# Kernel optimization log

Hardware: AMD Instinct MI355X
Metric: run time of the kernel (lower is better)

Reference implementation:

```python
import jax, jax.numpy as jnp
import numpy as np

N = 50000        # number of nodes
K = 32           # sampled neighbors per node (fixed degree)
D = 128          # input_dim
DOUT = 128       # output_dim


def setup_inputs() -> dict:
    key = jax.random.key(0)
    k1, k2, k3, k4, k5 = jax.random.split(key, 5)
    node_fea1 = jax.random.normal(k1, (N, D), dtype=jnp.float32)
    node_fea2 = jax.random.normal(k2, (N, D), dtype=jnp.float32)
    neigh_idx1 = jax.random.randint(k3, (N, K), 0, N, dtype=jnp.int32)
    neigh_idx2 = jax.random.randint(k4, (N, K), 0, N, dtype=jnp.int32)
    # xavier-uniform init for weight [4*D, DOUT]
    limit = float(np.sqrt(6.0 / (4 * D + DOUT)))
    weight = jax.random.uniform(k5, (4 * D, DOUT), dtype=jnp.float32,
                                minval=-limit, maxval=limit)
    return {"node_fea1": node_fea1, "node_fea2": node_fea2,
            "neigh_idx1": neigh_idx1, "neigh_idx2": neigh_idx2,
            "weight": weight}


def reference(node_fea1, node_fea2, neigh_idx1, neigh_idx2, weight):
    # neighbor mean aggregation of node_fea1 over the two neighbor lists
    # (forward_den reads node_fea1 in BOTH aggregation blocks)
    nei1 = node_fea1[neigh_idx1].mean(axis=1)   # [N, D]
    nei2 = node_fea1[neigh_idx2].mean(axis=1)   # [N, D]
    cat_fea = jnp.concatenate([node_fea1, node_fea2, nei1, nei2], axis=1)  # [N, 4D]
    return jnp.tanh(cat_fea @ weight)           # [N, DOUT]
```

## Files before the change

kernel.cpp:

```cpp
#include <hip/hip_runtime.h>
#include <math.h>

#define N_NODES 50000
#define KNEI    32
#define DIM     128
#define DOUT    128
#define NUNITS  (2 * N_NODES)

typedef __attribute__((ext_vector_type(8))) short short8;
typedef __attribute__((ext_vector_type(4))) float floatx4;
typedef __attribute__((ext_vector_type(4))) int  intx4;

static __device__ __forceinline__ unsigned short f2bf(float f) {
    unsigned int u = __float_as_uint(f);
    unsigned int lsb = (u >> 16) & 1u;
    u += 0x7fffu + lsb;
    return (unsigned short)(u >> 16);
}
static __device__ __forceinline__ unsigned int pack2(float a, float b) {
    return (unsigned int)f2bf(a) | ((unsigned int)f2bf(b) << 16);
}
static __device__ __forceinline__ float fast_tanh(float x) {
    float ax = fabsf(x);
    float e  = __expf(2.0f * ax);
    float t  = 1.0f - 2.0f / (e + 1.0f);
    return copysignf(t, x);
}
static __device__ __forceinline__ unsigned int pk4_u8(float a, float b, float c,
                                                      float d, float inv) {
    int qa = ((int)rintf(a * inv) + 128) & 0xff;
    int qb = ((int)rintf(b * inv) + 128) & 0xff;
    int qc = ((int)rintf(c * inv) + 128) & 0xff;
    int qd = ((int)rintf(d * inv) + 128) & 0xff;
    return (unsigned int)(qa | (qb << 8) | (qc << 16) | (qd << 24));
}


__global__ __launch_bounds__(256) void convert_both(
    const float* __restrict__ fea1, const float* __restrict__ W,
    unsigned char* __restrict__ Q8, float* __restrict__ Sc,
    unsigned short* __restrict__ Wt)
{
    int b = blockIdx.x;
    if (b >= 1563) {
        int t = (b - 1563) * 256 + threadIdx.x;
        int k = t >> 7, n = t & 127;
        Wt[n * 512 + k] = f2bf(W[t]);
        return;
    }
    int t = b * 256 + threadIdx.x;
    if (t >= N_NODES * 8) return;
    int node = t >> 3, j = t & 7;
    const float* rp = fea1 + node * DIM + j * 16;
    float4 v0 = *(const float4*)rp;
    float4 v1 = *(const float4*)(rp + 4);
    float4 v2 = *(const float4*)(rp + 8);
    float4 v3 = *(const float4*)(rp + 12);

    float am = fabsf(v0.x);
    am = fmaxf(am, fabsf(v0.y)); am = fmaxf(am, fabsf(v0.z)); am = fmaxf(am, fabsf(v0.w));
    am = fmaxf(am, fabsf(v1.x)); am = fmaxf(am, fabsf(v1.y));
    am = fmaxf(am, fabsf(v1.z)); am = fmaxf(am, fabsf(v1.w));
    am = fmaxf(am, fabsf(v2.x)); am = fmaxf(am, fabsf(v2.y));
    am = fmaxf(am, fabsf(v2.z)); am = fmaxf(am, fabsf(v2.w));
    am = fmaxf(am, fabsf(v3.x)); am = fmaxf(am, fabsf(v3.y));
    am = fmaxf(am, fabsf(v3.z)); am = fmaxf(am, fabsf(v3.w));
    #pragma unroll
    for (int d = 1; d < 8; d <<= 1) am = fmaxf(am, __shfl_xor(am, d, 64));

    float inv = (am > 1e-30f) ? 127.0f / am : 0.0f;
    uint4 o;
    o.x = pk4_u8(v0.x, v0.y, v0.z, v0.w, inv);
    o.y = pk4_u8(v1.x, v1.y, v1.z, v1.w, inv);
    o.z = pk4_u8(v2.x, v2.y, v2.z, v2.w, inv);
    o.w = pk4_u8(v3.x, v3.y, v3.z, v3.w, inv);
    unsigned char* qp = Q8 + (size_t)(j >> 2) * (N_NODES * 64)
                           + (size_t)node * 64 + (j & 3) * 16;
    *(uint4*)qp = o;
    if (j == 0) Sc[node] = am * (1.0f / 127.0f);
}

__global__ __launch_bounds__(256) void aggregate_plane(
    const unsigned char* __restrict__ Q8,
    const float* __restrict__ Sc,
    const int* __restrict__ idx1,
    const int* __restrict__ idx2,
    unsigned short* __restrict__ NEI,
    const int plane)
{
    __shared__ int   idxs[64][36];
    __shared__ float scs[64][36];

    const int tid = threadIdx.x;
    const int bu0 = blockIdx.x * 64;
    const int ul  = tid >> 2;
    const int l   = tid & 3;

    #pragma unroll
    for (int i = 0; i < 2; ++i) {
        int s   = tid + i * 256;
        int us  = s >> 3;
        int off = (s & 7) * 4;
        int uu  = bu0 + us;
        if (uu >= NUNITS) uu = NUNITS - 1;
        const int* ip = ((uu & 1) ? idx2 : idx1) + (uu >> 1) * KNEI + off;
        intx4 v = __builtin_nontemporal_load((const intx4*)ip);
        *(intx4*)&idxs[us][off] = v;
    }
    __syncthreads();

    #pragma unroll
    for (int i = 0; i < 2; ++i) {
        int s   = tid + i * 256;
        int us  = s >> 3;
        int off = (s & 7) * 4;
        #pragma unroll
        for (int k = 0; k < 4; ++k)
            scs[us][off + k] = Sc[idxs[us][off + k]];
    }
    __syncthreads();

    const int u    = bu0 + ul;
    const int cu   = (u < NUNITS) ? u : (NUNITS - 1);
    const int node = cu >> 1;
    const int list = cu & 1;

    const unsigned char* qb = Q8 + (size_t)plane * (N_NODES * 64) + l * 16;
    float sums[16];
    #pragma unroll
    for (int i = 0; i < 16; ++i) sums[i] = 0.f;
    float ssum = 0.f;

    #pragma unroll 2
    for (int b = 0; b < 4; ++b) {
        int4 i4a = *(const int4*)&idxs[ul][b * 8];
        int4 i4b = *(const int4*)&idxs[ul][b * 8 + 4];
        int rows[8] = {i4a.x, i4a.y, i4a.z, i4a.w,
                       i4b.x, i4b.y, i4b.z, i4b.w};
        uint4 v[8];
        #pragma unroll
        for (int j = 0; j < 8; ++j)
            v[j] = *(const uint4*)(qb + (size_t)rows[j] * 64);

        float4 sA = *(const float4*)&scs[ul][b * 8];
        float4 sB = *(const float4*)&scs[ul][b * 8 + 4];
        float sc8[8] = {sA.x, sA.y, sA.z, sA.w, sB.x, sB.y, sB.z, sB.w};
        ssum += sA.x + sA.y + sA.z + sA.w + sB.x + sB.y + sB.z + sB.w;

        #pragma unroll
        for (int j = 0; j < 8; ++j) {
            float s = sc8[j];
            unsigned int d0 = v[j].x, d1 = v[j].y, d2 = v[j].z, d3 = v[j].w;
            sums[0]  = fmaf(s, (float)(d0 & 0xffu),         sums[0]);
            sums[1]  = fmaf(s, (float)((d0 >> 8) & 0xffu),  sums[1]);
            sums[2]  = fmaf(s, (float)((d0 >> 16) & 0xffu), sums[2]);
            sums[3]  = fmaf(s, (float)(d0 >> 24),           sums[3]);
            sums[4]  = fmaf(s, (float)(d1 & 0xffu),         sums[4]);
            sums[5]  = fmaf(s, (float)((d1 >> 8) & 0xffu),  sums[5]);
            sums[6]  = fmaf(s, (float)((d1 >> 16) & 0xffu), sums[6]);
            sums[7]  = fmaf(s, (float)(d1 >> 24),           sums[7]);
            sums[8]  = fmaf(s, (float)(d2 & 0xffu),         sums[8]);
            sums[9]  = fmaf(s, (float)((d2 >> 8) & 0xffu),  sums[9]);
            sums[10] = fmaf(s, (float)((d2 >> 16) & 0xffu), sums[10]);
            sums[11] = fmaf(s, (float)(d2 >> 24),           sums[11]);
            sums[12] = fmaf(s, (float)(d3 & 0xffu),         sums[12]);
            sums[13] = fmaf(s, (float)((d3 >> 8) & 0xffu),  sums[13]);
            sums[14] = fmaf(s, (float)((d3 >> 16) & 0xffu), sums[14]);
            sums[15] = fmaf(s, (float)(d3 >> 24),           sums[15]);
        }
    }

    const float invK = 1.0f / 32.0f;
    const float corr = 128.0f * ssum;
    #pragma unroll
    for (int i = 0; i < 16; ++i) sums[i] = (sums[i] - corr) * invK;

    if (u < NUNITS) {
        intx4 o0, o1;
        o0.x = (int)pack2(sums[0],  sums[1]);
        o0.y = (int)pack2(sums[2],  sums[3]);
        o0.z = (int)pack2(sums[4],  sums[5]);
        o0.w = (int)pack2(sums[6],  sums[7]);
        o1.x = (int)pack2(sums[8],  sums[9]);
        o1.y = (int)pack2(sums[10], sums[11]);
        o1.z = (int)pack2(sums[12], sums[13]);
        o1.w = (int)pack2(sums[14], sums[15]);
        unsigned short* op = NEI + node * 256 + list * 128 + plane * 64 + l * 16;
        __builtin_nontemporal_store(o0, (intx4*)op);
        __builtin_nontemporal_store(o1, (intx4*)(op + 8));
    }
}

__global__ __launch_bounds__(256) void gemm128(
    const float*          __restrict__ fea1,
    const float*          __restrict__ fea2,
    const unsigned short* __restrict__ NEI,
    const unsigned short* __restrict__ Wt,
    float* __restrict__ out)
{
    __shared__ unsigned short As[128][72];
    __shared__ unsigned short Bs[128][72];

    const int tid  = threadIdx.x;
    const int w    = tid >> 6;
    const int lane = tid & 63;
    const int m0   = blockIdx.x * 128;
    const int wm   = (w & 1) * 64;
    const int wn   = (w >> 1) * 64;
    const int lm   = lane & 15;
    const int lk   = (lane >> 4) * 8;

    floatx4 acc[4][4];
    #pragma unroll
    for (int i = 0; i < 4; ++i)
        #pragma unroll
        for (int j = 0; j < 4; ++j)
            acc[i][j] = (floatx4){0.f, 0.f, 0.f, 0.f};

    for (int cc = 0; cc < 8; ++cc) {
        const int kb = cc * 64;
        if (cc < 4) {
            const float* src = (cc < 2) ? fea1 : fea2;
            const int cbase = (cc & 1) * 64;
            #pragma unroll
            for (int i = 0; i < 8; ++i) {
                int f   = tid + i * 256;
                int row = f >> 4;
                int c4  = (f & 15) * 4;
                int node = m0 + row;
                if (node >= N_NODES) node = N_NODES - 1;
                float4 v = *(const float4*)(src + node * DIM + cbase + c4);
                *(unsigned int*)&As[row][c4 + 0] = pack2(v.x, v.y);
                *(unsigned int*)&As[row][c4 + 2] = pack2(v.z, v.w);
            }
        } else {
            const int cb = kb - 256;
            #pragma unroll
            for (int i = 0; i < 4; ++i) {
                int sl  = tid + i * 256;
                int row = sl >> 3;
                int o8  = (sl & 7) * 8;
                int node = m0 + row;
                if (node >= N_NODES) node = N_NODES - 1;
                *(int4*)&As[row][o8] = *(const int4*)(NEI + node * 256 + cb + o8);
            }
        }
        #pragma unroll
        for (int i = 0; i < 4; ++i) {
            int sl  = tid + i * 256;
            int row = sl >> 3;
            int o8  = (sl & 7) * 8;
            *(int4*)&Bs[row][o8] = *(const int4*)(Wt + row * 512 + kb + o8);
        }
        __syncthreads();

        #pragma unroll
        for (int ks = 0; ks < 64; ks += 32) {
            short8 af[4], bf_[4];
            #pragma unroll
            for (int im = 0; im < 4; ++im)
                af[im] = *(const short8*)&As[wm + im * 16 + lm][ks + lk];
            #pragma unroll
            for (int in = 0; in < 4; ++in)
                bf_[in] = *(const short8*)&Bs[wn + in * 16 + lm][ks + lk];
            #pragma unroll
            for (int im = 0; im < 4; ++im)
                #pragma unroll
                for (int in = 0; in < 4; ++in)
                    acc[im][in] = __builtin_amdgcn_mfma_f32_16x16x32_bf16(
                        af[im], bf_[in], acc[im][in], 0, 0, 0);
        }
        __syncthreads();
    }

    #pragma unroll
    for (int im = 0; im < 4; ++im) {
        int rbase = m0 + wm + im * 16 + (lane >> 4) * 4;
        #pragma unroll
        for (int in = 0; in < 4; ++in) {
            int col = wn + in * 16 + lm;
            #pragma unroll
            for (int r = 0; r < 4; ++r) {
                int node = rbase + r;
                if (node < N_NODES)
                    out[node * DOUT + col] = fast_tanh(acc[im][in][r]);
            }
        }
    }
}

#define MT      64
#define KC      64
#define AS_STRIDE 68

__global__ __launch_bounds__(256) void sage_fused_fb(
    const float* __restrict__ fea1, const float* __restrict__ fea2,
    const int* __restrict__ idx1, const int* __restrict__ idx2,
    const float* __restrict__ W, float* __restrict__ out)
{
    __shared__ float As[KC][AS_STRIDE];
    __shared__ int   idxs[MT][64];
    const int tid = threadIdx.x;
    const int n0  = blockIdx.x * MT;
    #pragma unroll
    for (int i = 0; i < 8; ++i) {
        int e = tid + i * 256, m = e >> 5, kk = e & 31;
        int node = n0 + m; if (node >= N_NODES) node = N_NODES - 1;
        idxs[m][kk]      = idx1[node * KNEI + kk];
        idxs[m][32 + kk] = idx2[node * KNEI + kk];
    }
    float acc[8][4];
    #pragma unroll
    for (int i = 0; i < 8; ++i)
        #pragma unroll
        for (int j = 0; j < 4; ++j) acc[i][j] = 0.f;
    const int j0 = (tid & 31) * 4;
    const int m0 = (tid >> 5) * 8;
    for (int c = 0; c < 8; ++c) {
        if (c < 4) {
            const float* src = (c < 2) ? fea1 : fea2;
            const int cbase = (c & 1) * 64;
            #pragma unroll
            for (int i = 0; i < 4; ++i) {
                int f = tid + i * 256, m = f >> 4, c4 = (f & 15) * 4;
                int node = n0 + m; if (node >= N_NODES) node = N_NODES - 1;
                float4 v = *(const float4*)(src + node * DIM + cbase + c4);
                As[c4 + 0][m] = v.x; As[c4 + 1][m] = v.y;
                As[c4 + 2][m] = v.z; As[c4 + 3][m] = v.w;
            }
        } else {
            const int col = tid & 63, kbase = (c & 1) * 64;
            const int lbase = (c < 6) ? 0 : 32, g = tid >> 6;
            for (int mm = 0; mm < 16; ++mm) {
                const int m = g * 16 + mm;
                const int4* ip = (const int4*)&idxs[m][lbase];
                float s = 0.f;
                #pragma unroll
                for (int q = 0; q < 8; ++q) {
                    int4 nb = ip[q];
                    s += fea1[nb.x * DIM + kbase + col];
                    s += fea1[nb.y * DIM + kbase + col];
                    s += fea1[nb.z * DIM + kbase + col];
                    s += fea1[nb.w * DIM + kbase + col];
                }
                As[col][m] = s * (1.0f / 32.0f);
            }
        }
        __syncthreads();
        const float* wp = W + (c * KC) * DOUT + j0;
        #pragma unroll 4
        for (int k = 0; k < KC; ++k) {
            float4 w4 = *(const float4*)(wp + k * DOUT);
            const float4* ap = (const float4*)&As[k][m0];
            float4 a0 = ap[0]; float4 a1 = ap[1];
            float av[8] = {a0.x, a0.y, a0.z, a0.w, a1.x, a1.y, a1.z, a1.w};
            #pragma unroll
            for (int i = 0; i < 8; ++i) {
                acc[i][0] += av[i] * w4.x; acc[i][1] += av[i] * w4.y;
                acc[i][2] += av[i] * w4.z; acc[i][3] += av[i] * w4.w;
            }
        }
        __syncthreads();
    }
    #pragma unroll
    for (int i = 0; i < 8; ++i) {
        int node = n0 + m0 + i;
        if (node < N_NODES) {
            float4 r;
            r.x = tanhf(acc[i][0]); r.y = tanhf(acc[i][1]);
            r.z = tanhf(acc[i][2]); r.w = tanhf(acc[i][3]);
            *(float4*)(out + node * DOUT + j0) = r;
        }
    }
}

extern "C" void kernel_launch(void* const* d_in, const int* in_sizes, int n_in,
                              void* d_out, int out_size, void* d_ws, size_t ws_size,
                              hipStream_t stream) {
    const float* fea1 = (const float*)d_in[0];
    const float* fea2 = (const float*)d_in[1];
    const int*   idx1 = (const int*)d_in[2];
    const int*   idx2 = (const int*)d_in[3];
    const float* W    = (const float*)d_in[4];
    float* out = (float*)d_out;

    const size_t Q8_BYTES  = (size_t)N_NODES * DIM;
    const size_t SC_BYTES  = (size_t)N_NODES * 4;
    const size_t NEI_BYTES = (size_t)N_NODES * 256 * 2;
    const size_t WT_BYTES  = (size_t)512 * 128 * 2;

    if (ws_size >= Q8_BYTES + SC_BYTES + NEI_BYTES + WT_BYTES) {
        unsigned char*  Q8  = (unsigned char*)d_ws;
        float*          Scp = (float*)((char*)d_ws + Q8_BYTES);
        unsigned short* NEI = (unsigned short*)((char*)d_ws + Q8_BYTES + SC_BYTES);
        unsigned short* Wt  = (unsigned short*)((char*)d_ws + Q8_BYTES + SC_BYTES + NEI_BYTES);

        convert_both<<<1563 + 256, 256, 0, stream>>>(fea1, W, Q8, Scp, Wt);
        const int agrid = (NUNITS + 63) / 64;
        aggregate_plane<<<agrid, 256, 0, stream>>>(Q8, Scp, idx1, idx2, NEI, 0);
        aggregate_plane<<<agrid, 256, 0, stream>>>(Q8, Scp, idx1, idx2, NEI, 1);
        gemm128<<<(N_NODES + 127) / 128, 256, 0, stream>>>(fea1, fea2, NEI, Wt, out);
    } else {
        const int grid = (N_NODES + MT - 1) / MT;
        sage_fused_fb<<<grid, 256, 0, stream>>>(fea1, fea2, idx1, idx2, W, out);
    }
}
```

Measured before the change: 193.0 us.

## Store int8 features row-contiguous, aggregate in one pass, shrink GEMM tile

The quantized feature table changes from two 64-byte column planes to one contiguous 128-byte row per node. The two per-plane aggregation launches merge into a single 1024-thread kernel in which 8 lanes cover a full row, so each gathered neighbor row is fetched once and the indices and scales are read once. The GEMM tile shrinks from 128 to 64 rows to launch more blocks, at the cost of reloading the weight tile more often. The split plane layout had been an attempt to keep each plane cache-resident, and that benefit is given up here.

```diff
diff --git a/kernel.cpp b/kernel.cpp
--- a/kernel.cpp
+++ b/kernel.cpp
@@ -38,7 +38,7 @@
 
 __global__ __launch_bounds__(256) void convert_both(
     const float* __restrict__ fea1, const float* __restrict__ W,
-    unsigned char* __restrict__ Q8, float* __restrict__ Sc,
+    unsigned int* __restrict__ Q8, float* __restrict__ Sc,
     unsigned short* __restrict__ Wt)
 {
     int b = blockIdx.x;
@@ -69,38 +69,33 @@
     for (int d = 1; d < 8; d <<= 1) am = fmaxf(am, __shfl_xor(am, d, 64));
 
     float inv = (am > 1e-30f) ? 127.0f / am : 0.0f;
-    uint4 o;
-    o.x = pk4_u8(v0.x, v0.y, v0.z, v0.w, inv);
-    o.y = pk4_u8(v1.x, v1.y, v1.z, v1.w, inv);
-    o.z = pk4_u8(v2.x, v2.y, v2.z, v2.w, inv);
-    o.w = pk4_u8(v3.x, v3.y, v3.z, v3.w, inv);
-    unsigned char* qp = Q8 + (size_t)(j >> 2) * (N_NODES * 64)
-                           + (size_t)node * 64 + (j & 3) * 16;
-    *(uint4*)qp = o;
+    int4 o;
+    o.x = (int)pk4_u8(v0.x, v0.y, v0.z, v0.w, inv);
+    o.y = (int)pk4_u8(v1.x, v1.y, v1.z, v1.w, inv);
+    o.z = (int)pk4_u8(v2.x, v2.y, v2.z, v2.w, inv);
+    o.w = (int)pk4_u8(v3.x, v3.y, v3.z, v3.w, inv);
+    *(int4*)(Q8 + node * 32 + j * 4) = o;
     if (j == 0) Sc[node] = am * (1.0f / 127.0f);
 }
 
-__global__ __launch_bounds__(256) void aggregate_plane(
+__global__ __launch_bounds__(1024) void aggregate_i8(
     const unsigned char* __restrict__ Q8,
     const float* __restrict__ Sc,
     const int* __restrict__ idx1,
     const int* __restrict__ idx2,
-    unsigned short* __restrict__ NEI,
-    const int plane)
+    unsigned short* __restrict__ NEI)
 {
-    __shared__ int   idxs[64][36];
-    __shared__ float scs[64][36];
+    __shared__ int   idxs[128][40];
+    __shared__ float scs[128][40];
 
     const int tid = threadIdx.x;
-    const int bu0 = blockIdx.x * 64;
-    const int ul  = tid >> 2;
-    const int l   = tid & 3;
-
-    #pragma unroll
-    for (int i = 0; i < 2; ++i) {
-        int s   = tid + i * 256;
-        int us  = s >> 3;
-        int off = (s & 7) * 4;
+    const int bu0 = blockIdx.x * 128;
+    const int ul  = tid >> 3;
+    const int l   = tid & 7;
+
+    {
+        int us  = tid >> 3;
+        int off = (tid & 7) * 4;
         int uu  = bu0 + us;
         if (uu >= NUNITS) uu = NUNITS - 1;
         const int* ip = ((uu & 1) ? idx2 : idx1) + (uu >> 1) * KNEI + off;
@@ -109,14 +104,10 @@
     }
     __syncthreads();
 
-    #pragma unroll
-    for (int i = 0; i < 2; ++i) {
-        int s   = tid + i * 256;
-        int us  = s >> 3;
-        int off = (s & 7) * 4;
+    {
         #pragma unroll
         for (int k = 0; k < 4; ++k)
-            scs[us][off + k] = Sc[idxs[us][off + k]];
+            scs[ul][l * 4 + k] = Sc[idxs[ul][l * 4 + k]];
     }
     __syncthreads();
 
@@ -125,7 +116,7 @@
     const int node = cu >> 1;
     const int list = cu & 1;
 
-    const unsigned char* qb = Q8 + (size_t)plane * (N_NODES * 64) + l * 16;
+    const unsigned char* base = Q8 + l * 16;
     float sums[16];
     #pragma unroll
     for (int i = 0; i < 16; ++i) sums[i] = 0.f;
@@ -140,7 +131,7 @@
         uint4 v[8];
         #pragma unroll
         for (int j = 0; j < 8; ++j)
-            v[j] = *(const uint4*)(qb + (size_t)rows[j] * 64);
+            v[j] = *(const uint4*)(base + (size_t)rows[j] * 128);
 
         float4 sA = *(const float4*)&scs[ul][b * 8];
         float4 sB = *(const float4*)&scs[ul][b * 8 + 4];
@@ -185,34 +176,34 @@
         o1.y = (int)pack2(sums[10], sums[11]);
         o1.z = (int)pack2(sums[12], sums[13]);
         o1.w = (int)pack2(sums[14], sums[15]);
-        unsigned short* op = NEI + node * 256 + list * 128 + plane * 64 + l * 16;
+        unsigned short* op = NEI + node * 256 + list * 128 + l * 16;
         __builtin_nontemporal_store(o0, (intx4*)op);
         __builtin_nontemporal_store(o1, (intx4*)(op + 8));
     }
 }
 
-__global__ __launch_bounds__(256) void gemm128(
+__global__ __launch_bounds__(256) void gemm64(
     const float*          __restrict__ fea1,
     const float*          __restrict__ fea2,
     const unsigned short* __restrict__ NEI,
     const unsigned short* __restrict__ Wt,
     float* __restrict__ out)
 {
-    __shared__ unsigned short As[128][72];
+    __shared__ unsigned short As[64][72];
     __shared__ unsigned short Bs[128][72];
 
     const int tid  = threadIdx.x;
     const int w    = tid >> 6;
     const int lane = tid & 63;
-    const int m0   = blockIdx.x * 128;
-    const int wm   = (w & 1) * 64;
+    const int m0   = blockIdx.x * 64;
+    const int wm   = (w & 1) * 32;
     const int wn   = (w >> 1) * 64;
     const int lm   = lane & 15;
     const int lk   = (lane >> 4) * 8;
 
-    floatx4 acc[4][4];
-    #pragma unroll
-    for (int i = 0; i < 4; ++i)
+    floatx4 acc[2][4];
+    #pragma unroll
+    for (int i = 0; i < 2; ++i)
         #pragma unroll
         for (int j = 0; j < 4; ++j)
             acc[i][j] = (floatx4){0.f, 0.f, 0.f, 0.f};
@@ -223,7 +214,7 @@
             const float* src = (cc < 2) ? fea1 : fea2;
             const int cbase = (cc & 1) * 64;
             #pragma unroll
-            for (int i = 0; i < 8; ++i) {
+            for (int i = 0; i < 2; ++i) {
                 int f   = tid + i * 256;
                 int row = f >> 4;
                 int c4  = (f & 15) * 4;
@@ -233,10 +224,21 @@
                 *(unsigned int*)&As[row][c4 + 0] = pack2(v.x, v.y);
                 *(unsigned int*)&As[row][c4 + 2] = pack2(v.z, v.w);
             }
+            #pragma unroll
+            for (int i = 2; i < 4; ++i) {
+                int f   = tid + i * 256;
+                int row = f >> 4;
+                int c4  = (f & 15) * 4;
+                int node = m0 + row;
+                if (node >= N_NODES) node = N_NODES - 1;
+                float4 v = *(const float4*)(src + node * DIM + cbase + c4);
+                *(unsigned int*)&As[row][c4 + 0] = pack2(v.x, v.y);
+                *(unsigned int*)&As[row][c4 + 2] = pack2(v.z, v.w);
+            }
         } else {
             const int cb = kb - 256;
             #pragma unroll
-            for (int i = 0; i < 4; ++i) {
+            for (int i = 0; i < 2; ++i) {
                 int sl  = tid + i * 256;
                 int row = sl >> 3;
                 int o8  = (sl & 7) * 8;
@@ -256,15 +258,15 @@
 
         #pragma unroll
         for (int ks = 0; ks < 64; ks += 32) {
-            short8 af[4], bf_[4];
-            #pragma unroll
-            for (int im = 0; im < 4; ++im)
+            short8 af[2], bf_[4];
+            #pragma unroll
+            for (int im = 0; im < 2; ++im)
                 af[im] = *(const short8*)&As[wm + im * 16 + lm][ks + lk];
             #pragma unroll
             for (int in = 0; in < 4; ++in)
                 bf_[in] = *(const short8*)&Bs[wn + in * 16 + lm][ks + lk];
             #pragma unroll
-            for (int im = 0; im < 4; ++im)
+            for (int im = 0; im < 2; ++im)
                 #pragma unroll
                 for (int in = 0; in < 4; ++in)
                     acc[im][in] = __builtin_amdgcn_mfma_f32_16x16x32_bf16(
@@ -274,7 +276,7 @@
     }
 
     #pragma unroll
-    for (int im = 0; im < 4; ++im) {
+    for (int im = 0; im < 2; ++im) {
         int rbase = m0 + wm + im * 16 + (lane >> 4) * 4;
         #pragma unroll
         for (int in = 0; in < 4; ++in) {
@@ -395,11 +397,11 @@
         unsigned short* NEI = (unsigned short*)((char*)d_ws + Q8_BYTES + SC_BYTES);
         unsigned short* Wt  = (unsigned short*)((char*)d_ws + Q8_BYTES + SC_BYTES + NEI_BYTES);
 
-        convert_both<<<1563 + 256, 256, 0, stream>>>(fea1, W, Q8, Scp, Wt);
-        const int agrid = (NUNITS + 63) / 64;
-        aggregate_plane<<<agrid, 256, 0, stream>>>(Q8, Scp, idx1, idx2, NEI, 0);
-        aggregate_plane<<<agrid, 256, 0, stream>>>(Q8, Scp, idx1, idx2, NEI, 1);
-        gemm128<<<(N_NODES + 127) / 128, 256, 0, stream>>>(fea1, fea2, NEI, Wt, out);
+        convert_both<<<1563 + 256, 256, 0, stream>>>(
+            fea1, W, (unsigned int*)Q8, Scp, Wt);
+        aggregate_i8<<<(NUNITS + 127) / 128, 1024, 0, stream>>>(
+            Q8, Scp, idx1, idx2, NEI);
+        gemm64<<<(N_NODES + 63) / 64, 256, 0, stream>>>(fea1, fea2, NEI, Wt, out);
     } else {
         const int grid = (N_NODES + MT - 1) / MT;
         sage_fused_fb<<<grid, 256, 0, stream>>>(fea1, fea2, idx1, idx2, W, out);
```

Result: faster. 182.4 us (-5.5%).
